# Performance work log

Hardware: AMD Instinct MI355X
Metric: run time of the kernel (lower is better)

The kernel has to match this reference:

```python
import jax, jax.numpy as jnp
import numpy as np

N = 100000        # number of nodes
E = 1600000       # number of edges (avg degree 16)
D_IN = 512
D_OUT = 64


def setup_inputs() -> dict:
    key = jax.random.key(0)
    k1, k2, k3, k4, k5 = jax.random.split(key, 5)
    inputs = jax.random.normal(k1, (N, D_IN), dtype=jnp.float32)
    weight = jax.random.normal(k2, (D_IN, D_OUT), dtype=jnp.float32)
    adj_vals = jax.random.uniform(k3, (E,), dtype=jnp.float32)
    adj_rows = jax.random.randint(k4, (E,), 0, N, dtype=jnp.int32)
    adj_cols = jax.random.randint(k5, (E,), 0, N, dtype=jnp.int32)
    return {
        "inputs": inputs,
        "weight": weight,
        "adj_vals": adj_vals,
        "adj_rows": adj_rows,
        "adj_cols": adj_cols,
    }


def reference(inputs, weight, adj_vals, adj_rows, adj_cols):
    # Dense projection: [N, D_IN] @ [D_IN, D_OUT] -> [N, D_OUT]
    h = inputs @ weight
    # Sparse adjacency spmm (COO): out[r] += vals[e] * h[c] for edge e=(r,c)
    msgs = adj_vals[:, None] * h[adj_cols]            # [E, D_OUT]
    agg = jax.ops.segment_sum(msgs, adj_rows, num_segments=N)  # [N, D_OUT]
    # activation = relu
    return jax.nn.relu(agg)
```

## Files before the change

### kernel.cpp

```cpp
#include <hip/hip_runtime.h>
#include <hip/hip_bf16.h>

#define D_OUT 64
#define K_DIM 512
#define RPB 128
#define RPB_SHIFT 7
#define EPB 8192
#define GCAP 3072
#define RCAP 3072
#define CPAD 16

using short8  = __attribute__((ext_vector_type(8))) short;
using floatx4 = __attribute__((ext_vector_type(4))) float;

__device__ inline unsigned short f32_to_bf16(float f) {
    __hip_bfloat16 b = __float2bfloat16(f);
    return *reinterpret_cast<unsigned short*>(&b);
}

__device__ inline unsigned int pk_bf16(float lo, float hi) {
    __hip_bfloat162 p = __float22bfloat162_rn(make_float2(lo, hi));
    return *reinterpret_cast<unsigned int*>(&p);
}

__device__ inline float bf16lo_f32(unsigned int g) {
    return __uint_as_float(g << 16);
}
__device__ inline float bf16hi_f32(unsigned int g) {
    return __uint_as_float(g & 0xFFFF0000u);
}

__global__ void wt_kernel(const float* __restrict__ W, unsigned short* __restrict__ wt) {
    int i = blockIdx.x * blockDim.x + threadIdx.x;
    if (i < D_OUT * K_DIM) {
        int n = i >> 9;
        int k = i & 511;
        wt[i] = f32_to_bf16(W[k * D_OUT + n]);
    }
}

__global__ __launch_bounds__(256) void gemm_kernel(
    const float* __restrict__ A, const unsigned short* __restrict__ wt,
    unsigned short* __restrict__ H, int n) {
    const int tid  = threadIdx.x;
    const int wv   = tid >> 6;
    const int lane = tid & 63;
    const int ln   = lane & 15;
    const int quad = lane >> 4;
    const int row0 = blockIdx.x * 64 + wv * 16;

    int arow = row0 + ln;
    if (arow >= n) arow = n - 1;
    const float* Arow = A + (size_t)arow * K_DIM;
    const unsigned short* wb = wt + (size_t)ln * K_DIM;

    floatx4 acc0 = {0.f, 0.f, 0.f, 0.f};
    floatx4 acc1 = {0.f, 0.f, 0.f, 0.f};
    floatx4 acc2 = {0.f, 0.f, 0.f, 0.f};
    floatx4 acc3 = {0.f, 0.f, 0.f, 0.f};

    for (int h0 = 0; h0 < K_DIM; h0 += 128) {
        float4 t[8];
#pragma unroll
        for (int s = 0; s < 4; s++) {
            t[2 * s]     = *reinterpret_cast<const float4*>(Arow + h0 + s * 32 + quad * 8);
            t[2 * s + 1] = *reinterpret_cast<const float4*>(Arow + h0 + s * 32 + quad * 8 + 4);
        }
        short8 ab[4];
#pragma unroll
        for (int s = 0; s < 4; s++) {
            float4 a0 = t[2 * s], a1 = t[2 * s + 1];
            int4 pk;
            pk.x = (int)pk_bf16(a0.x, a0.y);
            pk.y = (int)pk_bf16(a0.z, a0.w);
            pk.z = (int)pk_bf16(a1.x, a1.y);
            pk.w = (int)pk_bf16(a1.z, a1.w);
            ab[s] = *reinterpret_cast<short8*>(&pk);
        }
#pragma unroll
        for (int s = 0; s < 4; s++) {
            const int ko = h0 + s * 32 + quad * 8;
            short8 b0 = *reinterpret_cast<const short8*>(wb + ko);
            short8 b1 = *reinterpret_cast<const short8*>(wb + 16 * K_DIM + ko);
            short8 b2 = *reinterpret_cast<const short8*>(wb + 32 * K_DIM + ko);
            short8 b3 = *reinterpret_cast<const short8*>(wb + 48 * K_DIM + ko);
            acc0 = __builtin_amdgcn_mfma_f32_16x16x32_bf16(ab[s], b0, acc0, 0, 0, 0);
            acc1 = __builtin_amdgcn_mfma_f32_16x16x32_bf16(ab[s], b1, acc1, 0, 0, 0);
            acc2 = __builtin_amdgcn_mfma_f32_16x16x32_bf16(ab[s], b2, acc2, 0, 0, 0);
            acc3 = __builtin_amdgcn_mfma_f32_16x16x32_bf16(ab[s], b3, acc3, 0, 0, 0);
        }
    }

#pragma unroll
    for (int r = 0; r < 4; r++) {
        int gr = row0 + quad * 4 + r;
        if (gr < n) {
            unsigned short* Hr = H + (size_t)gr * D_OUT;
            Hr[ln]      = f32_to_bf16(acc0[r]);
            Hr[16 + ln] = f32_to_bf16(acc1[r]);
            Hr[32 + ln] = f32_to_bf16(acc2[r]);
            Hr[48 + ln] = f32_to_bf16(acc3[r]);
        }
    }
}

__global__ __launch_bounds__(256) void init_kernel(int* __restrict__ cursor, int nbuck) {
    int b = blockIdx.x * 256 + threadIdx.x;
    if (b < nbuck) cursor[b * CPAD] = b * GCAP;
}

__global__ __launch_bounds__(256) void part_kernel(
    const int* __restrict__ rows, const int* __restrict__ cols,
    const float* __restrict__ vals, int* __restrict__ cursor,
    int2* __restrict__ keys, int E, int nbuck) {
    extern __shared__ int sm[];
    int* cnt  = sm;
    int* offs = sm + nbuck;
    const int tid = threadIdx.x, blk = blockIdx.x;

    for (int b = tid; b < nbuck; b += 256) cnt[b] = 0;
    __syncthreads();

    const int base = blk * EPB;
#pragma unroll
    for (int i = 0; i < EPB / 256; i++) {
        int e = base + tid + i * 256;
        if (e < E) atomicAdd(&cnt[rows[e] >> RPB_SHIFT], 1);
    }
    __syncthreads();

    for (int b = tid; b < nbuck; b += 256) {
        int c = cnt[b];
        offs[b] = c ? atomicAdd(&cursor[b * CPAD], c) : 0;
    }
    __syncthreads();

#pragma unroll
    for (int i = 0; i < EPB / 256; i++) {
        int e = base + tid + i * 256;
        if (e < E) {
            int r = rows[e];
            int c = cols[e];
            float v = vals[e];
            int b = r >> RPB_SHIFT;
            int p = atomicAdd(&offs[b], 1);
            if (p < (b + 1) * GCAP)
                keys[p] = make_int2(c | ((r & (RPB - 1)) << 17), __float_as_int(v));
        }
    }
}

__global__ __launch_bounds__(512) void sort_agg_kernel(
    const unsigned short* __restrict__ h, const int2* __restrict__ keys,
    const int* __restrict__ cursor, float* __restrict__ out, int N) {
    __shared__ int2 rec[RCAP];
    __shared__ int cnt[RPB];
    __shared__ int excl[RPB];
    __shared__ int cur[RPB];
    __shared__ int wtot[2];

    const int tid  = threadIdx.x;
    const int lane = tid & 63;
    const int wv   = tid >> 6;
    const int q    = lane >> 4;
    const int li   = lane & 15;
    const int b    = blockIdx.x;

    const int start = b * GCAP;
    int m = cursor[b * CPAD] - start;
    if (m > GCAP) m = GCAP;

    if (tid < RPB) cnt[tid] = 0;
    __syncthreads();

    for (int i = tid; i < m; i += 512) {
        int rl = keys[start + i].x >> 17;
        atomicAdd(&cnt[rl], 1);
    }
    __syncthreads();

    int v = 0, x = 0;
    if (tid < RPB) {
        v = cnt[tid];
        x = v;
#pragma unroll
        for (int d = 1; d < 64; d <<= 1) {
            int y = __shfl_up(x, d, 64);
            if (lane >= d) x += y;
        }
        if (lane == 63) wtot[tid >> 6] = x;
    }
    __syncthreads();
    if (tid < RPB) {
        int base = (tid >= 64) ? wtot[0] : 0;
        int ex = base + x - v;
        excl[tid] = ex;
        cur[tid]  = ex;
    }
    __syncthreads();

    for (int i = tid; i < m; i += 512) {
        int2 kv = keys[start + i];
        int rl = kv.x >> 17;
        int p = atomicAdd(&cur[rl], 1);
        if (p < RCAP) rec[p] = kv;
    }
    __syncthreads();

    const int row0 = b * RPB;
    for (int rl = wv; rl < RPB; rl += 8) {
        int s = excl[rl];
        int e = cur[rl];
        float4 acc = {0.f, 0.f, 0.f, 0.f};
        int j = s;
        for (; j + 8 <= e; j += 8) {
            int2 kA = rec[j + q];
            int2 kB = rec[j + 4 + q];
            const uint2 gA = *reinterpret_cast<const uint2*>(
                h + (size_t)(kA.x & 0x1FFFF) * D_OUT + li * 4);
            const uint2 gB = *reinterpret_cast<const uint2*>(
                h + (size_t)(kB.x & 0x1FFFF) * D_OUT + li * 4);
            float vA = __int_as_float(kA.y);
            float vB = __int_as_float(kB.y);
            acc.x += vA * bf16lo_f32(gA.x);
            acc.y += vA * bf16hi_f32(gA.x);
            acc.z += vA * bf16lo_f32(gA.y);
            acc.w += vA * bf16hi_f32(gA.y);
            acc.x += vB * bf16lo_f32(gB.x);
            acc.y += vB * bf16hi_f32(gB.x);
            acc.z += vB * bf16lo_f32(gB.y);
            acc.w += vB * bf16hi_f32(gB.y);
        }
        for (; j < e; j += 4) {
            bool on = (j + q) < e;
            int2 kv = rec[on ? j + q : j];
            const uint2 g = *reinterpret_cast<const uint2*>(
                h + (size_t)(kv.x & 0x1FFFF) * D_OUT + li * 4);
            float vv = on ? __int_as_float(kv.y) : 0.f;
            acc.x += vv * bf16lo_f32(g.x);
            acc.y += vv * bf16hi_f32(g.x);
            acc.z += vv * bf16lo_f32(g.y);
            acc.w += vv * bf16hi_f32(g.y);
        }
        acc.x += __shfl_xor(acc.x, 16, 64);
        acc.y += __shfl_xor(acc.y, 16, 64);
        acc.z += __shfl_xor(acc.z, 16, 64);
        acc.w += __shfl_xor(acc.w, 16, 64);
        acc.x += __shfl_xor(acc.x, 32, 64);
        acc.y += __shfl_xor(acc.y, 32, 64);
        acc.z += __shfl_xor(acc.z, 32, 64);
        acc.w += __shfl_xor(acc.w, 32, 64);

        if (q == 0) {
            int gr = row0 + rl;
            if (gr < N) {
                float4 o;
                o.x = fmaxf(acc.x, 0.f);
                o.y = fmaxf(acc.y, 0.f);
                o.z = fmaxf(acc.z, 0.f);
                o.w = fmaxf(acc.w, 0.f);
                *reinterpret_cast<float4*>(out + (size_t)gr * D_OUT + li * 4) = o;
            }
        }
    }
}

extern "C" void kernel_launch(void* const* d_in, const int* in_sizes, int n_in,
                              void* d_out, int out_size, void* d_ws, size_t ws_size,
                              hipStream_t stream) {
    const float* A    = (const float*)d_in[0];
    const float* W    = (const float*)d_in[1];
    const float* vals = (const float*)d_in[2];
    const int*   rows = (const int*)d_in[3];
    const int*   cols = (const int*)d_in[4];
    float* out = (float*)d_out;

    const int N = out_size / D_OUT;
    const int E = in_sizes[2];
    const int nbuck = (N + RPB - 1) >> RPB_SHIFT;
    const int nb = (E + EPB - 1) / EPB;

    char* ws = (char*)d_ws;
    unsigned short* h      = (unsigned short*)ws;
    int2*           keys   = (int2*)(ws + (size_t)N * D_OUT * 2);
    unsigned short* wt     = (unsigned short*)((char*)keys + (size_t)nbuck * GCAP * 8);
    int*            cursor = (int*)((char*)wt + (size_t)D_OUT * K_DIM * 2);

    const size_t part_lds = (size_t)nbuck * 4 * 2;

    wt_kernel<<<(D_OUT * K_DIM + 255) / 256, 256, 0, stream>>>(W, wt);
    gemm_kernel<<<(N + 63) / 64, 256, 0, stream>>>(A, wt, h, N);
    init_kernel<<<(nbuck + 255) / 256, 256, 0, stream>>>(cursor, nbuck);
    part_kernel<<<nb, 256, part_lds, stream>>>(rows, cols, vals, cursor, keys, E, nbuck);
    sort_agg_kernel<<<nbuck, 512, 0, stream>>>(h, keys, cursor, out, N);
}
```

Measured before the change: 410.9 us.

## Stage partitioned edges in LDS for coalesced bucket writes; fold cursor init

The partition kernel now counting-sorts each 8192-edge chunk by bucket in shared memory: a block-wide scan gives per-bucket offsets, records are scattered into LDS, and a final pass writes them to global keys in bucket-contiguous runs instead of scattered 8-byte writes. Cursor initialization moves into the weight-transpose kernel, removing one launch. The static LDS use grows to roughly 100KB per block, which lowers occupancy, and NBK=1024 caps nbuck (782 here).

Result: no change. 405.8 us (-1.3%).

```diff
diff --git a/kernel.cpp b/kernel.cpp
--- a/kernel.cpp
+++ b/kernel.cpp
@@ -9,6 +9,7 @@
 #define GCAP 3072
 #define RCAP 3072
 #define CPAD 16
+#define NBK 1024
 
 using short8  = __attribute__((ext_vector_type(8))) short;
 using floatx4 = __attribute__((ext_vector_type(4))) float;
@@ -30,13 +31,15 @@
     return __uint_as_float(g & 0xFFFF0000u);
 }
 
-__global__ void wt_kernel(const float* __restrict__ W, unsigned short* __restrict__ wt) {
+__global__ void wt_kernel(const float* __restrict__ W, unsigned short* __restrict__ wt,
+                          int* __restrict__ cursor, int nbuck) {
     int i = blockIdx.x * blockDim.x + threadIdx.x;
     if (i < D_OUT * K_DIM) {
         int n = i >> 9;
         int k = i & 511;
         wt[i] = f32_to_bf16(W[k * D_OUT + n]);
     }
+    if (i < nbuck) cursor[i * CPAD] = i * GCAP;
 }
 
 __global__ __launch_bounds__(256) void gemm_kernel(
@@ -104,49 +107,80 @@
     }
 }
 
-__global__ __launch_bounds__(256) void init_kernel(int* __restrict__ cursor, int nbuck) {
-    int b = blockIdx.x * 256 + threadIdx.x;
-    if (b < nbuck) cursor[b * CPAD] = b * GCAP;
-}
-
 __global__ __launch_bounds__(256) void part_kernel(
     const int* __restrict__ rows, const int* __restrict__ cols,
     const float* __restrict__ vals, int* __restrict__ cursor,
     int2* __restrict__ keys, int E, int nbuck) {
-    extern __shared__ int sm[];
-    int* cnt  = sm;
-    int* offs = sm + nbuck;
-    const int tid = threadIdx.x, blk = blockIdx.x;
+    __shared__ int2 rec[EPB];
+    __shared__ unsigned short bkt[EPB];
+    __shared__ int cnt[NBK];
+    __shared__ int excl[NBK];
+    __shared__ int goff[NBK];
+    __shared__ int wsum[4];
+
+    const int tid = threadIdx.x, lane = tid & 63, wid = tid >> 6;
+    const int base = blockIdx.x * EPB;
+    int m = E - base; if (m > EPB) m = EPB;
 
     for (int b = tid; b < nbuck; b += 256) cnt[b] = 0;
     __syncthreads();
 
-    const int base = blk * EPB;
-#pragma unroll
-    for (int i = 0; i < EPB / 256; i++) {
-        int e = base + tid + i * 256;
-        if (e < E) atomicAdd(&cnt[rows[e] >> RPB_SHIFT], 1);
+    for (int i = tid; i < m; i += 256)
+        atomicAdd(&cnt[rows[base + i] >> RPB_SHIFT], 1);
+    __syncthreads();
+
+    int v[4];
+#pragma unroll
+    for (int j = 0; j < 4; j++) {
+        int ix = tid * 4 + j;
+        v[j] = (ix < nbuck) ? cnt[ix] : 0;
+    }
+#pragma unroll
+    for (int j = 1; j < 4; j++) v[j] += v[j - 1];
+    int t4 = v[3], x = t4;
+#pragma unroll
+    for (int d = 1; d < 64; d <<= 1) {
+        int y = __shfl_up(x, d, 64);
+        if (lane >= d) x += y;
+    }
+    if (lane == 63) wsum[wid] = x;
+    __syncthreads();
+    if (tid == 0) {
+        int a = 0;
+#pragma unroll
+        for (int w = 0; w < 4; w++) { int tt = wsum[w]; wsum[w] = a; a += tt; }
+    }
+    __syncthreads();
+    int ex0 = wsum[wid] + (x - t4);
+#pragma unroll
+    for (int j = 0; j < 4; j++) {
+        int ix = tid * 4 + j;
+        if (ix < nbuck) excl[ix] = ex0 + ((j == 0) ? 0 : v[j - 1]);
     }
     __syncthreads();
 
     for (int b = tid; b < nbuck; b += 256) {
         int c = cnt[b];
-        offs[b] = c ? atomicAdd(&cursor[b * CPAD], c) : 0;
-    }
-    __syncthreads();
-
-#pragma unroll
-    for (int i = 0; i < EPB / 256; i++) {
-        int e = base + tid + i * 256;
-        if (e < E) {
-            int r = rows[e];
-            int c = cols[e];
-            float v = vals[e];
-            int b = r >> RPB_SHIFT;
-            int p = atomicAdd(&offs[b], 1);
-            if (p < (b + 1) * GCAP)
-                keys[p] = make_int2(c | ((r & (RPB - 1)) << 17), __float_as_int(v));
-        }
+        goff[b] = c ? atomicAdd(&cursor[b * CPAD], c) : 0;
+        cnt[b] = excl[b];
+    }
+    __syncthreads();
+
+    for (int i = tid; i < m; i += 256) {
+        int r = rows[base + i];
+        int b = r >> RPB_SHIFT;
+        int p = atomicAdd(&cnt[b], 1);
+        rec[p] = make_int2(cols[base + i] | ((r & (RPB - 1)) << 17),
+                           __float_as_int(vals[base + i]));
+        bkt[p] = (unsigned short)b;
+    }
+    __syncthreads();
+
+    for (int i = tid; i < m; i += 256) {
+        int b = bkt[i];
+        int p = goff[b] + (i - excl[b]);
+        if (p < (b + 1) * GCAP)
+            keys[p] = rec[i];
     }
 }
 
@@ -286,11 +320,8 @@
     unsigned short* wt     = (unsigned short*)((char*)keys + (size_t)nbuck * GCAP * 8);
     int*            cursor = (int*)((char*)wt + (size_t)D_OUT * K_DIM * 2);
 
-    const size_t part_lds = (size_t)nbuck * 4 * 2;
-
-    wt_kernel<<<(D_OUT * K_DIM + 255) / 256, 256, 0, stream>>>(W, wt);
+    wt_kernel<<<(D_OUT * K_DIM + 255) / 256, 256, 0, stream>>>(W, wt, cursor, nbuck);
     gemm_kernel<<<(N + 63) / 64, 256, 0, stream>>>(A, wt, h, N);
-    init_kernel<<<(nbuck + 255) / 256, 256, 0, stream>>>(cursor, nbuck);
-    part_kernel<<<nb, 256, part_lds, stream>>>(rows, cols, vals, cursor, keys, E, nbuck);
+    part_kernel<<<nb, 256, 0, stream>>>(rows, cols, vals, cursor, keys, E, nbuck);
     sort_agg_kernel<<<nbuck, 512, 0, stream>>>(h, keys, cursor, out, N);
 }
```

## Fuse edge partitioning into GEMM launch and fold cursor init into weight transpose

Applied to the files above, without the earlier changes.

The edge-bucketing (partition) work is merged into the GEMM kernel as extra leading blocks, so the bandwidth-bound partition and the compute-bound projection run concurrently in one launch. The cursor initialization is folded into the weight-transpose kernel, removing two kernel launches. The cost is a fixed static LDS allocation (2*1024 ints) in every GEMM block, which can lower occupancy, and a hard limit of 1024 buckets.

New measurement: 384.3 us. 6.5% less time.

```diff
diff --git a/kernel.cpp b/kernel.cpp
--- a/kernel.cpp
+++ b/kernel.cpp
@@ -9,6 +9,7 @@
 #define GCAP 3072
 #define RCAP 3072
 #define CPAD 16
+#define NBK 1024
 
 using short8  = __attribute__((ext_vector_type(8))) short;
 using floatx4 = __attribute__((ext_vector_type(4))) float;
@@ -30,24 +31,71 @@
     return __uint_as_float(g & 0xFFFF0000u);
 }
 
-__global__ void wt_kernel(const float* __restrict__ W, unsigned short* __restrict__ wt) {
+__global__ void wt_kernel(const float* __restrict__ W, unsigned short* __restrict__ wt,
+                          int* __restrict__ cursor, int nbuck) {
     int i = blockIdx.x * blockDim.x + threadIdx.x;
     if (i < D_OUT * K_DIM) {
         int n = i >> 9;
         int k = i & 511;
         wt[i] = f32_to_bf16(W[k * D_OUT + n]);
     }
-}
-
-__global__ __launch_bounds__(256) void gemm_kernel(
+    if (i < nbuck) cursor[i * CPAD] = i * GCAP;
+}
+
+__global__ __launch_bounds__(256) void gemm_part_kernel(
     const float* __restrict__ A, const unsigned short* __restrict__ wt,
-    unsigned short* __restrict__ H, int n) {
-    const int tid  = threadIdx.x;
+    unsigned short* __restrict__ H, int n,
+    const int* __restrict__ rows, const int* __restrict__ cols,
+    const float* __restrict__ vals, int* __restrict__ cursor,
+    int2* __restrict__ keys, int E, int nbuck, int npart) {
+    __shared__ int sm[2 * NBK];
+
+    const int tid = threadIdx.x;
+
+    if (blockIdx.x < npart) {
+        int* cnt  = sm;
+        int* offs = sm + NBK;
+        const int blk = blockIdx.x;
+
+        for (int b = tid; b < nbuck; b += 256) cnt[b] = 0;
+        __syncthreads();
+
+        const int base = blk * EPB;
+#pragma unroll
+        for (int i = 0; i < EPB / 256; i++) {
+            int e = base + tid + i * 256;
+            if (e < E) atomicAdd(&cnt[rows[e] >> RPB_SHIFT], 1);
+        }
+        __syncthreads();
+
+        for (int b = tid; b < nbuck; b += 256) {
+            int c = cnt[b];
+            offs[b] = c ? atomicAdd(&cursor[b * CPAD], c) : 0;
+        }
+        __syncthreads();
+
+#pragma unroll
+        for (int i = 0; i < EPB / 256; i++) {
+            int e = base + tid + i * 256;
+            if (e < E) {
+                int r = rows[e];
+                int c = cols[e];
+                float v = vals[e];
+                int b = r >> RPB_SHIFT;
+                int p = atomicAdd(&offs[b], 1);
+                if (p < (b + 1) * GCAP)
+                    keys[p] = make_int2(c | ((r & (RPB - 1)) << 17), __float_as_int(v));
+            }
+        }
+        return;
+    }
+
+    const int gb   = blockIdx.x - npart;
     const int wv   = tid >> 6;
     const int lane = tid & 63;
     const int ln   = lane & 15;
     const int quad = lane >> 4;
-    const int row0 = blockIdx.x * 64 + wv * 16;
+    const int row0 = gb * 64 + wv * 16;
 
     int arow = row0 + ln;
     if (arow >= n) arow = n - 1;
@@ -100,52 +148,6 @@
             Hr[16 + ln] = f32_to_bf16(acc1[r]);
             Hr[32 + ln] = f32_to_bf16(acc2[r]);
             Hr[48 + ln] = f32_to_bf16(acc3[r]);
-        }
-    }
-}
-
-__global__ __launch_bounds__(256) void init_kernel(int* __restrict__ cursor, int nbuck) {
-    int b = blockIdx.x * 256 + threadIdx.x;
-    if (b < nbuck) cursor[b * CPAD] = b * GCAP;
-}
-
-__global__ __launch_bounds__(256) void part_kernel(
-    const int* __restrict__ rows, const int* __restrict__ cols,
-    const float* __restrict__ vals, int* __restrict__ cursor,
-    int2* __restrict__ keys, int E, int nbuck) {
-    extern __shared__ int sm[];
-    int* cnt  = sm;
-    int* offs = sm + nbuck;
-    const int tid = threadIdx.x, blk = blockIdx.x;
-
-    for (int b = tid; b < nbuck; b += 256) cnt[b] = 0;
-    __syncthreads();
-
-    const int base = blk * EPB;
-#pragma unroll
-    for (int i = 0; i < EPB / 256; i++) {
-        int e = base + tid + i * 256;
-        if (e < E) atomicAdd(&cnt[rows[e] >> RPB_SHIFT], 1);
-    }
-    __syncthreads();
-
-    for (int b = tid; b < nbuck; b += 256) {
-        int c = cnt[b];
-        offs[b] = c ? atomicAdd(&cursor[b * CPAD], c) : 0;
-    }
-    __syncthreads();
-
-#pragma unroll
-    for (int i = 0; i < EPB / 256; i++) {
-        int e = base + tid + i * 256;
-        if (e < E) {
-            int r = rows[e];
-            int c = cols[e];
-            float v = vals[e];
-            int b = r >> RPB_SHIFT;
-            int p = atomicAdd(&offs[b], 1);
-            if (p < (b + 1) * GCAP)
-                keys[p] = make_int2(c | ((r & (RPB - 1)) << 17), __float_as_int(v));
         }
     }
 }
@@ -279,6 +281,7 @@
     const int E = in_sizes[2];
     const int nbuck = (N + RPB - 1) >> RPB_SHIFT;
     const int nb = (E + EPB - 1) / EPB;
+    const int gb = (N + 63) / 64;
 
     char* ws = (char*)d_ws;
     unsigned short* h      = (unsigned short*)ws;
@@ -286,11 +289,9 @@
     unsigned short* wt     = (unsigned short*)((char*)keys + (size_t)nbuck * GCAP * 8);
     int*            cursor = (int*)((char*)wt + (size_t)D_OUT * K_DIM * 2);
 
-    const size_t part_lds = (size_t)nbuck * 4 * 2;
-
-    wt_kernel<<<(D_OUT * K_DIM + 255) / 256, 256, 0, stream>>>(W, wt);
-    gemm_kernel<<<(N + 63) / 64, 256, 0, stream>>>(A, wt, h, N);
-    init_kernel<<<(nbuck + 255) / 256, 256, 0, stream>>>(cursor, nbuck);
-    part_kernel<<<nb, 256, part_lds, stream>>>(rows, cols, vals, cursor, keys, E, nbuck);
+    wt_kernel<<<(D_OUT * K_DIM + 255) / 256, 256, 0, stream>>>(W, wt, cursor, nbuck);
+    gemm_part_kernel<<<nb + gb, 256, 0, stream>>>(A, wt, h, N,
+                                                  rows, cols, vals, cursor, keys,
+                                                  E, nbuck, nb);
     sort_agg_kernel<<<nbuck, 512, 0, stream>>>(h, keys, cursor, out, N);
 }
```
